# Performance work log

Hardware: AMD Instinct MI355X
Metric: run time of the kernel (lower is better)

Reference implementation:

```python
import jax, jax.numpy as jnp
import numpy as np


def _lstm_layer(x, Wih, Whh, bih, bhh):
    # x: (B, S, I); Wih: (4H, I); Whh: (4H, H)
    B, S, _ = x.shape
    H = Whh.shape[1]
    # Big batched GEMM for all input projections at once.
    xproj = jnp.einsum('bsi,gi->bsg', x, Wih) + bih + bhh  # (B, S, 4H)
    xproj_t = jnp.transpose(xproj, (1, 0, 2))              # (S, B, 4H)

    def step(carry, xp):
        h, c = carry
        gates = xp + h @ Whh.T                             # (B, 4H)
        i, f, g, o = jnp.split(gates, 4, axis=-1)          # torch gate order i,f,g,o
        i = jax.nn.sigmoid(i)
        f = jax.nn.sigmoid(f)
        g = jnp.tanh(g)
        o = jax.nn.sigmoid(o)
        c = f * c + i * g
        h = o * jnp.tanh(c)
        return (h, c), h

    h0 = jnp.zeros((B, H), dtype=x.dtype)
    c0 = jnp.zeros((B, H), dtype=x.dtype)
    (_, _), hs = jax.lax.scan(step, (h0, c0), xproj_t)     # hs: (S, B, H)
    return jnp.transpose(hs, (1, 0, 2))                    # (B, S, H)


def setup_inputs() -> dict:
    key = jax.random.key(0)
    ks = jax.random.split(key, 12)
    B, S, I, H, O = 64, 512, 512, 1024, 64
    s_in = 1.0 / np.sqrt(H)
    inp = {
        'x': jax.random.normal(ks[0], (B, S, I), dtype=jnp.float32),
        'Wih0': jax.random.uniform(ks[1], (4 * H, I), minval=-s_in, maxval=s_in),
        'Whh0': jax.random.uniform(ks[2], (4 * H, H), minval=-s_in, maxval=s_in),
        'bih0': jax.random.uniform(ks[3], (4 * H,), minval=-s_in, maxval=s_in),
        'bhh0': jax.random.uniform(ks[4], (4 * H,), minval=-s_in, maxval=s_in),
        'Wih1': jax.random.uniform(ks[5], (4 * H, H), minval=-s_in, maxval=s_in),
        'Whh1': jax.random.uniform(ks[6], (4 * H, H), minval=-s_in, maxval=s_in),
        'bih1': jax.random.uniform(ks[7], (4 * H,), minval=-s_in, maxval=s_in),
        'bhh1': jax.random.uniform(ks[8], (4 * H,), minval=-s_in, maxval=s_in),
        'Wfc': jax.random.uniform(ks[9], (O, H), minval=-s_in, maxval=s_in),
        'bfc': jax.random.uniform(ks[10], (O,), minval=-s_in, maxval=s_in),
    }
    return inp


def reference(x, Wih0, Whh0, bih0, bhh0, Wih1, Whh1, bih1, bhh1, Wfc, bfc):
    h = _lstm_layer(x, Wih0, Whh0, bih0, bhh0)   # (B, S, H)
    h = _lstm_layer(h, Wih1, Whh1, bih1, bhh1)   # (B, S, H)
    # dropout = 0.0 (eval mode) -> identity
    logits = jnp.einsum('bsh,oh->bso', h, Wfc) + bfc  # (B, S, O)
    return logits
```

## Files before the change

### kernel.cpp

```cpp
#include <hip/hip_runtime.h>
#include <stdint.h>

typedef _Float16 f16;
typedef _Float16 f16x8 __attribute__((ext_vector_type(8)));
typedef float f32x4 __attribute__((ext_vector_type(4)));

#define MFMA16(a, b, c) __builtin_amdgcn_mfma_f32_16x16x32_f16((a), (b), (c), 0, 0, 0)



__global__ void k_conv_x(const float* __restrict__ x, f16* __restrict__ x16) {
  int i = blockIdx.x * 256 + threadIdx.x;
  int o = i * 8;
  int s = o >> 15, b = (o >> 9) & 63, c = o & 511;
  const float* src = x + (size_t)b * 262144 + (size_t)s * 512 + c;
  float4 v0 = *(const float4*)(src);
  float4 v1 = *(const float4*)(src + 4);
  union { f16 h[8]; f16x8 v; } t;
  t.h[0] = (f16)v0.x; t.h[1] = (f16)v0.y; t.h[2] = (f16)v0.z; t.h[3] = (f16)v0.w;
  t.h[4] = (f16)v1.x; t.h[5] = (f16)v1.y; t.h[6] = (f16)v1.z; t.h[7] = (f16)v1.w;
  *(f16x8*)(x16 + o) = t.v;
}

__global__ void k_conv_wfrag(const float* __restrict__ Wih, const float* __restrict__ Whh,
                             f16* __restrict__ Wf, int KI, int KK, int mode) {
  int fid = blockIdx.x;
  int lane = threadIdx.x;
  int cf = fid & 3; int rest = fid >> 2;
  int kk = rest % KK; rest /= KK; int w = rest & 7; int jc = rest >> 3;
  int c = cf * 16 + (lane & 15);
  int g = (c >> 4) * 1024 + jc * 16 + (c & 15);
  int k = (mode == 0)
              ? ((kk < 2) ? (w * 64 + kk * 32) : (512 + w * 128 + (kk - 2) * 32))
              : (w * 256 + kk * 32);
  k += (lane >> 4) << 3;
  const float* src = (k < KI) ? (Wih + (size_t)g * KI + k)
                              : (Whh + (size_t)g * 1024 + (k - KI));
  union { f16 h[8]; f16x8 v; } t;
#pragma unroll
  for (int i = 0; i < 8; ++i) t.h[i] = (f16)src[i];
  *(f16x8*)(Wf + ((size_t)fid * 64 + lane) * 8) = t.v;
}

__global__ void k_conv_bias(const float* __restrict__ bih, const float* __restrict__ bhh,
                            float* __restrict__ br) {
  int d = blockIdx.x * 64 + threadIdx.x;
  int jc = d >> 6, c = d & 63;
  int g = (c >> 4) * 1024 + jc * 16 + (c & 15);
  br[d] = bih[g] + bhh[g];
}

__global__ void k_conv_wfc(const float* __restrict__ Wfc, f16* __restrict__ Wfc16) {
  int i = blockIdx.x * 256 + threadIdx.x;
  Wfc16[i] = (f16)Wfc[i];
}

__global__ __attribute__((amdgpu_flat_work_group_size(512, 512), amdgpu_waves_per_eu(2, 2)))
void k_persist(const f16* __restrict__ x16,
               const f16* __restrict__ W0f, const float* __restrict__ b0r,
               const f16* __restrict__ W1f, const float* __restrict__ b1r,
               f16* __restrict__ h0buf, f16* __restrict__ h1buf,
               f16* __restrict__ h1all, unsigned char* flags8) {
  const int layer = blockIdx.x >> 7;
  const int sub = blockIdx.x & 127;
  const int rh = sub >> 6, jc = sub & 63;

  __shared__ float cred[8][32][66];

  unsigned char* myflag = flags8 + rh * 128 + layer * 64 + jc;

  const int tid = threadIdx.x;
  const int w = tid >> 6, lane = tid & 63;
  const int l15 = lane & 15, q8 = (lane >> 4) << 3;
  const int rbase = rh * 32;
  const int m = tid >> 4, jl = tid & 15;

  const float* bias = (layer ? b1r : b0r) + jc * 64;
  const float bI = bias[jl], bF = bias[16 + jl], bG = bias[32 + jl], bO = bias[48 + jl];
  float creg = 0.f;

#define POLLG(n0v, n1v)                                                                  \
  {                                                                                      \
    if (w == 0) {                                                                        \
      int li = lane & 31;                                                                \
      int needI = (li < 16) ? (n0v) : (n1v);                                             \
      if (needI < 0) needI = 0;                                                          \
      unsigned int nb = (unsigned int)needI & 255u;                                      \
      const unsigned int* fp_ = (const unsigned int*)(flags8 + rh * 128) + li;           \
      for (;;) {                                                                         \
        unsigned int v_;                                                                 \
        asm volatile("global_load_dword %0, %1, off sc0 sc1\n\ts_waitcnt vmcnt(0)"       \
                     : "=&v"(v_) : "v"(fp_) : "memory");                                 \
        unsigned int ok = (((v_ & 255u) - nb) & 255u) < 128u;                            \
        ok &= ((((v_ >> 8) & 255u) - nb) & 255u) < 128u;                                 \
        ok &= ((((v_ >> 16) & 255u) - nb) & 255u) < 128u;                                \
        ok &= ((((v_ >> 24) & 255u) - nb) & 255u) < 128u;                                \
        if (__all(ok)) break;                                                            \
        __builtin_amdgcn_s_sleep(1);                                                     \
      }                                                                                  \
    }                                                                                    \
    __syncthreads();                                                                     \
  }

#define CRED_AND_POINTWISE(HOUT, HALL)                                                   \
  {                                                                                      \
    _Pragma("unroll") for (int rf = 0; rf < 2; ++rf)                                     \
      _Pragma("unroll") for (int cf = 0; cf < 4; ++cf)                                   \
        _Pragma("unroll") for (int r = 0; r < 4; ++r)                                    \
          cred[w][rf * 16 + (lane >> 4) * 4 + r][cf * 16 + l15] = acc[rf][cf][r];        \
    __syncthreads();                                                                     \
    float ip = bI, fp = bF, gp2 = bG, op = bO;                                           \
    _Pragma("unroll") for (int ww = 0; ww < 8; ++ww) {                                   \
      ip += cred[ww][m][jl];                                                             \
      fp += cred[ww][m][16 + jl];                                                        \
      gp2 += cred[ww][m][32 + jl];                                                       \
      op += cred[ww][m][48 + jl];                                                        \
    }                                                                                    \
    float ig = 1.f / (1.f + __expf(-ip));                                                \
    float fg = 1.f / (1.f + __expf(-fp));                                                \
    float ea = __expf(-2.f * fabsf(gp2));                                                \
    float gg = copysignf((1.f - ea) / (1.f + ea), gp2);                                  \
    float og = 1.f / (1.f + __expf(-op));                                                \
    creg = fg * creg + ig * gg;                                                          \
    float eb = __expf(-2.f * fabsf(creg));                                               \
    float hval = og * copysignf((1.f - eb) / (1.f + eb), creg);                          \
    size_t idx = (size_t)(rbase + m) * 1024 + jc * 16 + jl;                              \
    union { f16 h; unsigned short s; } cv; cv.h = (f16)hval;                             \
    __hip_atomic_store((unsigned short*)((HOUT) + idx), cv.s,                            \
                       __ATOMIC_RELAXED, __HIP_MEMORY_SCOPE_AGENT);                      \
    if (HALL) ((f16*)(HALL))[idx] = cv.h;                                                \
    __syncthreads();                   \
    if (tid == 0) {                                                                      \
      unsigned int fv = (unsigned int)(t + 1) & 255u;                                    \
      asm volatile("global_store_byte %0, %1, off sc0 sc1" ::                            \
                   "v"(myflag), "v"(fv) : "memory");                                     \
    }                                                                                    \
  }

#define GLD_X(dst, addr)                                                                 \
  asm volatile("global_load_dwordx4 %0, %1, off sc0 sc1" : "=&v"(dst) : "v"(addr) : "memory")
#define GLD_C(dst, addr)                                                                 \
  asm volatile("global_load_dwordx4 %0, %1, off" : "=&v"(dst) : "v"(addr) : "memory")
#define WAITV(n)                                                                         \
  { asm volatile("s_waitcnt vmcnt(" #n ")" ::: "memory"); __builtin_amdgcn_sched_barrier(0); }

  if (layer == 0) {
    const int KK = 6;
    f16x8 wreg[6][4];
#pragma unroll
    for (int kk = 0; kk < KK; ++kk)
#pragma unroll
      for (int cf = 0; cf < 4; ++cf)
        wreg[kk][cf] = *(const f16x8*)(W0f + ((size_t)((jc * 8 + w) * KK + kk) * 4 + cf) * 512 + lane * 8);
#pragma unroll
    for (int kk = 0; kk < KK; ++kk)
      asm volatile("" : "+v"(wreg[kk][0]), "+v"(wreg[kk][1]), "+v"(wreg[kk][2]), "+v"(wreg[kk][3]));

    for (int t = 0; t < 512; ++t) {
      const f16* A0x = x16 + (size_t)t * 32768;
      const f16* A1h = h0buf + (size_t)((t + 3) & 3) * 65536;
      f16* hout = h0buf + (size_t)(t & 3) * 65536;

      f16x8 af[6][2];
#define ISSUE_X(kk)                                                                      \
      {                                                                                  \
        int k_ = w * 64 + (kk) * 32 + q8;                                                \
        const f16* ap_ = A0x + k_;                                                       \
        GLD_C(af[kk][0], ap_ + (size_t)(rbase + l15) * 512);                             \
        GLD_C(af[kk][1], ap_ + (size_t)(rbase + 16 + l15) * 512);                        \
      }
#define ISSUE_H0(kk)                                                                     \
      {                                                                                  \
        int hk_ = w * 128 + ((kk) - 2) * 32 + q8;                                        \
        const f16* ap_ = A1h + hk_;                                                      \
        GLD_X(af[kk][0], ap_ + (size_t)(rbase + l15) * 1024);                            \
        GLD_X(af[kk][1], ap_ + (size_t)(rbase + 16 + l15) * 1024);                       \
      }
#define MF0(kk)                                                                          \
      { _Pragma("unroll") for (int rf = 0; rf < 2; ++rf)                                 \
          _Pragma("unroll") for (int cf = 0; cf < 4; ++cf)                               \
            acc[rf][cf] = MFMA16(af[kk][rf], wreg[kk][cf], acc[rf][cf]); }

      f32x4 acc[2][4];
#pragma unroll
      for (int i = 0; i < 2; ++i)
#pragma unroll
        for (int j = 0; j < 4; ++j) acc[i][j] = f32x4{0.f, 0.f, 0.f, 0.f};

      ISSUE_X(0) ISSUE_X(1)
      POLLG(t, t - 3);
      ISSUE_H0(2) ISSUE_H0(3) ISSUE_H0(4) ISSUE_H0(5)
      WAITV(8)  MF0(0) MF0(1)
      WAITV(6)  MF0(2)
      WAITV(4)  MF0(3)
      WAITV(2)  MF0(4)
      WAITV(0)  MF0(5)
#undef ISSUE_X
#undef ISSUE_H0
#undef MF0

      CRED_AND_POINTWISE(hout, (f16*)nullptr);
    }
  } else {
    const int KK = 8;
    f16x8 wreg[8][4];
#pragma unroll
    for (int kk = 0; kk < KK; ++kk)
#pragma unroll
      for (int cf = 0; cf < 4; ++cf)
        wreg[kk][cf] = *(const f16x8*)(W1f + ((size_t)((jc * 8 + w) * KK + kk) * 4 + cf) * 512 + lane * 8);
#pragma unroll
    for (int kk = 0; kk < KK; ++kk)
      asm volatile("" : "+v"(wreg[kk][0]), "+v"(wreg[kk][1]), "+v"(wreg[kk][2]), "+v"(wreg[kk][3]));

    const int kbeg = w * 256;
    for (int t = 0; t < 512; ++t) {
      const f16* A0 = h0buf + (size_t)(t & 3) * 65536;
      const f16* A1 = h1buf + (size_t)((t + 3) & 3) * 65536;
      f16* hout = h1buf + (size_t)(t & 3) * 65536;
      f16* hall = h1all + (size_t)t * 65536;

      POLLG(t + 1, t);

      f16x8 af[4][2];
#define ISSUE1(kk)                                                                       \
      {                                                                                  \
        int k_ = kbeg + (kk) * 32 + q8;                                                  \
        const f16* ap_ = (k_ < 1024) ? (A0 + k_) : (A1 + (k_ - 1024));                   \
        GLD_X(af[(kk) & 3][0], ap_ + (size_t)(rbase + l15) * 1024);                      \
        GLD_X(af[(kk) & 3][1], ap_ + (size_t)(rbase + 16 + l15) * 1024);                 \
      }
#define MF1(kk)                                                                          \
      { _Pragma("unroll") for (int rf = 0; rf < 2; ++rf)                                 \
          _Pragma("unroll") for (int cf = 0; cf < 4; ++cf)                               \
            acc[rf][cf] = MFMA16(af[(kk) & 3][rf], wreg[kk][cf], acc[rf][cf]); }

      f32x4 acc[2][4];
#pragma unroll
      for (int i = 0; i < 2; ++i)
#pragma unroll
        for (int j = 0; j < 4; ++j) acc[i][j] = f32x4{0.f, 0.f, 0.f, 0.f};

      ISSUE1(0) ISSUE1(1) ISSUE1(2) ISSUE1(3)
      WAITV(6) MF1(0) ISSUE1(4)
      WAITV(6) MF1(1) ISSUE1(5)
      WAITV(6) MF1(2) ISSUE1(6)
      WAITV(6) MF1(3) ISSUE1(7)
      WAITV(6) MF1(4)
      WAITV(4) MF1(5)
      WAITV(2) MF1(6)
      WAITV(0) MF1(7)
#undef ISSUE1
#undef MF1

      CRED_AND_POINTWISE(hout, hall);
    }
  }
#undef POLLG
#undef CRED_AND_POINTWISE
#undef GLD_X
#undef GLD_C
#undef WAITV
}

__global__ __launch_bounds__(512, 1)
void k_fc(const f16* __restrict__ h1all, const f16* __restrict__ Wfc16,
          const float* __restrict__ bfc, float* __restrict__ out) {
  const int s = blockIdx.x;
  const f16* A = h1all + (size_t)s * 65536;
  __shared__ float credf[8][64][68];

  const int w = threadIdx.x >> 6;
  const int lane = threadIdx.x & 63;
  const int l15 = lane & 15;
  const int ksub = (lane >> 4) << 3;

  f32x4 acc[4][4];
#pragma unroll
  for (int i = 0; i < 4; ++i)
#pragma unroll
    for (int j = 0; j < 4; ++j) acc[i][j] = f32x4{0.f, 0.f, 0.f, 0.f};

  const int kbeg = w * 128, kend = kbeg + 128;
  f16x8 af0[4], bf0[4], af1[4], bf1[4];

  auto LOADK = [&](int kc, f16x8(&a)[4], f16x8(&b)[4]) {
    const f16* ap = A + kc + ksub;
#pragma unroll
    for (int rf = 0; rf < 4; ++rf)
      a[rf] = *(const f16x8*)(ap + (size_t)(rf * 16 + l15) * 1024);
    const f16* bp = Wfc16 + kc + ksub;
#pragma unroll
    for (int cf = 0; cf < 4; ++cf)
      b[cf] = *(const f16x8*)(bp + (size_t)(cf * 16 + l15) * 1024);
  };

  LOADK(kbeg, af0, bf0);
  for (int kc = kbeg; kc < kend; kc += 64) {
    LOADK(kc + 32, af1, bf1);
#pragma unroll
    for (int rf = 0; rf < 4; ++rf)
#pragma unroll
      for (int cf = 0; cf < 4; ++cf) acc[rf][cf] = MFMA16(af0[rf], bf0[cf], acc[rf][cf]);
    if (kc + 64 < kend) LOADK(kc + 64, af0, bf0);
#pragma unroll
    for (int rf = 0; rf < 4; ++rf)
#pragma unroll
      for (int cf = 0; cf < 4; ++cf) acc[rf][cf] = MFMA16(af1[rf], bf1[cf], acc[rf][cf]);
  }

#pragma unroll
  for (int rf = 0; rf < 4; ++rf)
#pragma unroll
    for (int cf = 0; cf < 4; ++cf)
#pragma unroll
      for (int r = 0; r < 4; ++r)
        credf[w][rf * 16 + (lane >> 4) * 4 + r][cf * 16 + l15] = acc[rf][cf][r];

  __syncthreads();

  int m = threadIdx.x >> 3;
  int cbase = (threadIdx.x & 7) * 8;
#pragma unroll
  for (int u = 0; u < 8; ++u) {
    int col = cbase + u;
    float v = bfc[col];
#pragma unroll
    for (int ww = 0; ww < 8; ++ww) v += credf[ww][m][col];
    out[((size_t)m * 512 + s) * 64 + col] = v;
  }
}

extern "C" void kernel_launch(void* const* d_in, const int* in_sizes, int n_in,
                              void* d_out, int out_size, void* d_ws, size_t ws_size,
                              hipStream_t stream) {
  const float* x    = (const float*)d_in[0];
  const float* Wih0 = (const float*)d_in[1];
  const float* Whh0 = (const float*)d_in[2];
  const float* bih0 = (const float*)d_in[3];
  const float* bhh0 = (const float*)d_in[4];
  const float* Wih1 = (const float*)d_in[5];
  const float* Whh1 = (const float*)d_in[6];
  const float* bih1 = (const float*)d_in[7];
  const float* bhh1 = (const float*)d_in[8];
  const float* Wfc  = (const float*)d_in[9];
  const float* bfc  = (const float*)d_in[10];
  float* out = (float*)d_out;

  char* ws = (char*)d_ws;
  f16*   W0f   = (f16*)(ws + 0);
  f16*   W1f   = (f16*)(ws + 12582912);
  f16*   Wfc16 = (f16*)(ws + 29360128);
  float* b0r   = (float*)(ws + 29491200);
  float* b1r   = (float*)(ws + 29507584);
  f16*   x16   = (f16*)(ws + 29523968);
  f16*   h1all = (f16*)(ws + 63078400);
  f16*   h0buf = (f16*)(ws + 130187264);
  f16*   h1buf = (f16*)(ws + 130711552);
  unsigned char* flags8 = (unsigned char*)(ws + 131235840);

  k_conv_x<<<8192, 256, 0, stream>>>(x, x16);
  k_conv_wfrag<<<12288, 64, 0, stream>>>(Wih0, Whh0, W0f, 512, 6, 0);
  k_conv_wfrag<<<16384, 64, 0, stream>>>(Wih1, Whh1, W1f, 1024, 8, 1);
  k_conv_bias<<<64, 64, 0, stream>>>(bih0, bhh0, b0r);
  k_conv_bias<<<64, 64, 0, stream>>>(bih1, bhh1, b1r);
  k_conv_wfc<<<256, 256, 0, stream>>>(Wfc, Wfc16);
  hipMemsetAsync(ws + 130187264, 0, 524288 * 2 + 256, stream);

  {
    const f16* x16c = x16; const f16* W0fc = W0f; const float* b0rc = b0r;
    const f16* W1fc = W1f; const float* b1rc = b1r;
    f16 *p0 = h0buf, *p1 = h1buf, *ph = h1all;
    unsigned char* fl = flags8;
    void* kargs[] = { &x16c, &W0fc, &b0rc, &W1fc, &b1rc, &p0, &p1, &ph, &fl };
    hipLaunchCooperativeKernel((void*)k_persist, dim3(256), dim3(512), kargs, 0, stream);
  }

  k_fc<<<512, 512, 0, stream>>>(h1all, Wfc16, bfc, out);
}
```

Baseline: 4.837 ms.

## Deepen layer-0 h ring to 8 slots and write layer-1 h directly to history buffer

The layer-0 hidden-state ring grows from 4 to 8 slots, so layer 0 can run up to 7 steps ahead of layer 1 before it has to wait. Layer 1 now reads and writes its hidden state straight into a full-sequence ring buffer, which removes the separate duplicate store to h1all. The flag layout becomes layer-major, and a single wave polls all 64 flag dwords. The LDS reduction row is padded to 69 floats to change bank mapping. In exchange, each poll reads more flags and both wait conditions change.

```diff
diff --git a/kernel.cpp b/kernel.cpp
--- a/kernel.cpp
+++ b/kernel.cpp
@@ -59,15 +59,15 @@
 void k_persist(const f16* __restrict__ x16,
                const f16* __restrict__ W0f, const float* __restrict__ b0r,
                const f16* __restrict__ W1f, const float* __restrict__ b1r,
-               f16* __restrict__ h0buf, f16* __restrict__ h1buf,
-               f16* __restrict__ h1all, unsigned char* flags8) {
+               f16* __restrict__ h0buf, f16* __restrict__ h1ring,
+               unsigned char* flags8) {
   const int layer = blockIdx.x >> 7;
   const int sub = blockIdx.x & 127;
   const int rh = sub >> 6, jc = sub & 63;
 
-  __shared__ float cred[8][32][66];
-
-  unsigned char* myflag = flags8 + rh * 128 + layer * 64 + jc;
+  __shared__ float cred[8][32][69];
+
+  unsigned char* myflag = flags8 + layer * 128 + sub;
 
   const int tid = threadIdx.x;
   const int w = tid >> 6, lane = tid & 63;
@@ -82,11 +82,10 @@
 #define POLLG(n0v, n1v)                                                                  \
   {                                                                                      \
     if (w == 0) {                                                                        \
-      int li = lane & 31;                                                                \
-      int needI = (li < 16) ? (n0v) : (n1v);                                             \
+      int needI = (lane < 32) ? (n0v) : (n1v);                                           \
       if (needI < 0) needI = 0;                                                          \
       unsigned int nb = (unsigned int)needI & 255u;                                      \
-      const unsigned int* fp_ = (const unsigned int*)(flags8 + rh * 128) + li;           \
+      const unsigned int* fp_ = (const unsigned int*)flags8 + lane;                      \
       for (;;) {                                                                         \
         unsigned int v_;                                                                 \
         asm volatile("global_load_dword %0, %1, off sc0 sc1\n\ts_waitcnt vmcnt(0)"       \
@@ -102,7 +101,7 @@
     __syncthreads();                                                                     \
   }
 
-#define CRED_AND_POINTWISE(HOUT, HALL)                                                   \
+#define CRED_AND_POINTWISE(HOUT)                                                         \
   {                                                                                      \
     _Pragma("unroll") for (int rf = 0; rf < 2; ++rf)                                     \
       _Pragma("unroll") for (int cf = 0; cf < 4; ++cf)                                   \
@@ -128,8 +127,7 @@
     union { f16 h; unsigned short s; } cv; cv.h = (f16)hval;                             \
     __hip_atomic_store((unsigned short*)((HOUT) + idx), cv.s,                            \
                        __ATOMIC_RELAXED, __HIP_MEMORY_SCOPE_AGENT);                      \
-    if (HALL) ((f16*)(HALL))[idx] = cv.h;                                                \
-    __syncthreads();                   \
+    __syncthreads();                 \
     if (tid == 0) {                                                                      \
       unsigned int fv = (unsigned int)(t + 1) & 255u;                                    \
       asm volatile("global_store_byte %0, %1, off sc0 sc1" ::                            \
@@ -158,8 +156,8 @@
 
     for (int t = 0; t < 512; ++t) {
       const f16* A0x = x16 + (size_t)t * 32768;
-      const f16* A1h = h0buf + (size_t)((t + 3) & 3) * 65536;
-      f16* hout = h0buf + (size_t)(t & 3) * 65536;
+      const f16* A1h = h0buf + (size_t)((t + 7) & 7) * 65536;
+      f16* hout = h0buf + (size_t)(t & 7) * 65536;
 
       f16x8 af[6][2];
 #define ISSUE_X(kk)                                                                      \
@@ -188,7 +186,7 @@
         for (int j = 0; j < 4; ++j) acc[i][j] = f32x4{0.f, 0.f, 0.f, 0.f};
 
       ISSUE_X(0) ISSUE_X(1)
-      POLLG(t, t - 3);
+      POLLG(t, t - 7);
       ISSUE_H0(2) ISSUE_H0(3) ISSUE_H0(4) ISSUE_H0(5)
       WAITV(8)  MF0(0) MF0(1)
       WAITV(6)  MF0(2)
@@ -199,7 +197,7 @@
 #undef ISSUE_H0
 #undef MF0
 
-      CRED_AND_POINTWISE(hout, (f16*)nullptr);
+      CRED_AND_POINTWISE(hout);
     }
   } else {
     const int KK = 8;
@@ -215,10 +213,9 @@
 
     const int kbeg = w * 256;
     for (int t = 0; t < 512; ++t) {
-      const f16* A0 = h0buf + (size_t)(t & 3) * 65536;
-      const f16* A1 = h1buf + (size_t)((t + 3) & 3) * 65536;
-      f16* hout = h1buf + (size_t)(t & 3) * 65536;
-      f16* hall = h1all + (size_t)t * 65536;
+      const f16* A0 = h0buf + (size_t)(t & 7) * 65536;
+      const f16* A1 = h1ring + (size_t)t * 65536;
+      f16* hout = h1ring + (size_t)(t + 1) * 65536;
 
       POLLG(t + 1, t);
 
@@ -253,7 +250,7 @@
 #undef ISSUE1
 #undef MF1
 
-      CRED_AND_POINTWISE(hout, hall);
+      CRED_AND_POINTWISE(hout);
     }
   }
 #undef POLLG
@@ -348,16 +345,15 @@
   float* out = (float*)d_out;
 
   char* ws = (char*)d_ws;
-  f16*   W0f   = (f16*)(ws + 0);
-  f16*   W1f   = (f16*)(ws + 12582912);
-  f16*   Wfc16 = (f16*)(ws + 29360128);
-  float* b0r   = (float*)(ws + 29491200);
-  float* b1r   = (float*)(ws + 29507584);
-  f16*   x16   = (f16*)(ws + 29523968);
-  f16*   h1all = (f16*)(ws + 63078400);
-  f16*   h0buf = (f16*)(ws + 130187264);
-  f16*   h1buf = (f16*)(ws + 130711552);
-  unsigned char* flags8 = (unsigned char*)(ws + 131235840);
+  f16*   W0f    = (f16*)(ws + 0);
+  f16*   W1f    = (f16*)(ws + 12582912);
+  f16*   Wfc16  = (f16*)(ws + 29360128);
+  float* b0r    = (float*)(ws + 29491200);
+  float* b1r    = (float*)(ws + 29507584);
+  f16*   x16    = (f16*)(ws + 29523968);
+  f16*   h1ring = (f16*)(ws + 63078400);
+  f16*   h0buf  = (f16*)(ws + 130318336);
+  unsigned char* flags8 = (unsigned char*)(ws + 131366912);
 
   k_conv_x<<<8192, 256, 0, stream>>>(x, x16);
   k_conv_wfrag<<<12288, 64, 0, stream>>>(Wih0, Whh0, W0f, 512, 6, 0);
@@ -365,16 +361,17 @@
   k_conv_bias<<<64, 64, 0, stream>>>(bih0, bhh0, b0r);
   k_conv_bias<<<64, 64, 0, stream>>>(bih1, bhh1, b1r);
   k_conv_wfc<<<256, 256, 0, stream>>>(Wfc, Wfc16);
-  hipMemsetAsync(ws + 130187264, 0, 524288 * 2 + 256, stream);
+  hipMemsetAsync(ws + 63078400, 0, 131072, stream);
+  hipMemsetAsync(ws + 130318336, 0, 1048576 + 256, stream);
 
   {
     const f16* x16c = x16; const f16* W0fc = W0f; const float* b0rc = b0r;
     const f16* W1fc = W1f; const float* b1rc = b1r;
-    f16 *p0 = h0buf, *p1 = h1buf, *ph = h1all;
+    f16 *p0 = h0buf, *p1 = h1ring;
     unsigned char* fl = flags8;
-    void* kargs[] = { &x16c, &W0fc, &b0rc, &W1fc, &b1rc, &p0, &p1, &ph, &fl };
+    void* kargs[] = { &x16c, &W0fc, &b0rc, &W1fc, &b1rc, &p0, &p1, &fl };
     hipLaunchCooperativeKernel((void*)k_persist, dim3(256), dim3(512), kargs, 0, stream);
   }
 
-  k_fc<<<512, 512, 0, stream>>>(h1all, Wfc16, bfc, out);
-}
+  k_fc<<<512, 512, 0, stream>>>(h1ring + 65536, Wfc16, bfc, out);
+}
```

Result: faster. 4.689 ms (-3.1%).
